# Performance work log

Hardware: AMD Instinct MI355X
Metric: run time of the kernel (lower is better)

## Reference

```python
import jax, jax.numpy as jnp
import numpy as np

N = 8192       # num nodes
F_IN = 256     # num_features
NHID = 128     # nhid
E = 524288     # num edges (avg degree 64)
K = 32         # num_edge_preseve


def setup_inputs() -> dict:
    key = jax.random.key(0)
    ks = jax.random.split(key, 5)
    x = jax.random.normal(ks[0], (N, F_IN), jnp.float32)
    edge_index = jax.random.randint(ks[1], (2, E), 0, N, jnp.int32)
    W1 = jax.random.normal(ks[2], (F_IN, NHID), jnp.float32) / np.sqrt(F_IN)
    b1 = jnp.zeros((NHID,), jnp.float32)
    We = jax.random.normal(ks[3], (2 * NHID, 1), jnp.float32) / np.sqrt(2 * NHID)
    be = jnp.zeros((1,), jnp.float32)
    return {"x": x, "edge_index": edge_index, "W1": W1, "b1": b1, "We": We, "be": be}


def _segment_sparsemax(z, seg, num_segments):
    """Sparsemax applied independently within each segment (row) of an edge list."""
    E_ = z.shape[0]
    # group edges by segment, descending score within segment
    order = jnp.lexsort((-z, seg))
    zs = z[order]
    ss = seg[order]
    counts = jnp.zeros((num_segments,), jnp.int32).at[seg].add(1)
    starts = jnp.cumsum(counts) - counts                 # first sorted index of each segment
    pos = jnp.arange(E_, dtype=jnp.int32) - starts[ss]   # 0-based rank within segment
    cs = jnp.cumsum(zs)
    prefix = cs - zs                                     # cumsum excluding self
    seg_cs = cs - prefix[starts][ss]                     # within-segment inclusive cumsum
    j1 = (pos + 1).astype(zs.dtype)
    cond = 1.0 + j1 * zs > seg_cs                        # sparsemax support condition
    kmax = jax.ops.segment_max(jnp.where(cond, pos + 1, 0), ss, num_segments=num_segments)
    kmax = jnp.maximum(kmax, 1)                          # nonempty segments always have k>=1
    idx = jnp.clip(starts + kmax - 1, 0, E_ - 1)
    seg_cs_at_k = cs[idx] - prefix[jnp.clip(starts, 0, E_ - 1)]
    tau = (seg_cs_at_k - 1.0) / kmax.astype(zs.dtype)
    out_sorted = jnp.maximum(zs - tau[ss], 0.0)
    return jnp.zeros_like(z).at[order].set(out_sorted)


def reference(x, edge_index, W1, b1, We, be):
    h = jax.nn.relu(x @ W1 + b1)                 # [N, NHID]
    row, col = edge_index[0], edge_index[1]
    # edge score: Linear on concat([h[row], h[col]]) == split matmul (avoids [E, 2*NHID] concat)
    e = h[row] @ We[:NHID, 0] + h[col] @ We[NHID:, 0] + be[0]   # [E]
    scores = _segment_sparsemax(e, row, N)       # row-segmented sparsemax
    adj = jnp.zeros((N, N), h.dtype).at[row, col].set(scores)
    topv = jax.lax.top_k(adj, K)[0]              # [N, K], sorted descending
    thresh = topv[:, -1:]                        # per-row k-th largest value
    new_adj = jnp.where(adj >= thresh, adj, jnp.zeros((), adj.dtype))
    # original returns dense_to_sparse(new_adj) (data-dependent shape);
    # we return the equivalent masked dense adjacency.
    return h, new_adj
```

## Files before the change

kernel.cpp:

```cpp
#include <hip/hip_runtime.h>

#define N_    8192
#define FIN_  256
#define NHID_ 128
#define E_    524288
#define KTOP  32
#define CAP   160
#define HASHSZ 512

typedef unsigned short ushort_t;

__global__ __launch_bounds__(256) void k_fused(const float* __restrict__ x,
                                               const int* __restrict__ ei,
                                               const float* __restrict__ W1,
                                               const float* __restrict__ b1,
                                               const float* __restrict__ We,
                                               float* __restrict__ h,
                                               float* __restrict__ a,
                                               float* __restrict__ b,
                                               int* __restrict__ cnt,
                                               ushort_t* __restrict__ ecol) {
    __shared__ float xs[16][FIN_];
    int t = threadIdx.x;
    int blk = blockIdx.x;

    {
        int4 r4 = ((const int4*)ei)[blk * 256 + t];
        int4 c4 = ((const int4*)(ei + E_))[blk * 256 + t];
        int p;
        p = atomicAdd(&cnt[r4.x], 1); if (p < CAP) ecol[r4.x * CAP + p] = (ushort_t)c4.x;
        p = atomicAdd(&cnt[r4.y], 1); if (p < CAP) ecol[r4.y * CAP + p] = (ushort_t)c4.y;
        p = atomicAdd(&cnt[r4.z], 1); if (p < CAP) ecol[r4.z * CAP + p] = (ushort_t)c4.z;
        p = atomicAdd(&cnt[r4.w], 1); if (p < CAP) ecol[r4.w * CAP + p] = (ushort_t)c4.w;
    }

    int row0 = blk * 16;
    const float4* xg = (const float4*)(x + (size_t)row0 * FIN_);
    float4* xs4 = (float4*)&xs[0][0];
#pragma unroll
    for (int i = 0; i < 4; ++i) xs4[t + 256 * i] = xg[t + 256 * i];
    __syncthreads();

    int rg = t >> 5;
    int jg = t & 31;
    int r0 = 2 * rg, r1 = 2 * rg + 1;
    const float* wp = W1 + jg * 4;
    float4 bb = *(const float4*)(b1 + jg * 4);
    float4 acc0 = bb, acc1 = bb;
    const float* xr0 = xs[r0];
    const float* xr1 = xs[r1];
#pragma unroll 8
    for (int k = 0; k < FIN_; ++k) {
        float4 w = *(const float4*)(wp + (size_t)k * NHID_);
        float x0 = xr0[k], x1 = xr1[k];
        acc0.x = fmaf(x0, w.x, acc0.x);
        acc0.y = fmaf(x0, w.y, acc0.y);
        acc0.z = fmaf(x0, w.z, acc0.z);
        acc0.w = fmaf(x0, w.w, acc0.w);
        acc1.x = fmaf(x1, w.x, acc1.x);
        acc1.y = fmaf(x1, w.y, acc1.y);
        acc1.z = fmaf(x1, w.z, acc1.z);
        acc1.w = fmaf(x1, w.w, acc1.w);
    }
    acc0.x = fmaxf(acc0.x, 0.f); acc0.y = fmaxf(acc0.y, 0.f);
    acc0.z = fmaxf(acc0.z, 0.f); acc0.w = fmaxf(acc0.w, 0.f);
    acc1.x = fmaxf(acc1.x, 0.f); acc1.y = fmaxf(acc1.y, 0.f);
    acc1.z = fmaxf(acc1.z, 0.f); acc1.w = fmaxf(acc1.w, 0.f);
    *(float4*)(h + (size_t)(row0 + r0) * NHID_ + jg * 4) = acc0;
    *(float4*)(h + (size_t)(row0 + r1) * NHID_ + jg * 4) = acc1;

    float4 we1 = *(const float4*)(We + jg * 4);
    float4 we2 = *(const float4*)(We + NHID_ + jg * 4);
    float p0 = acc0.x * we1.x + acc0.y * we1.y + acc0.z * we1.z + acc0.w * we1.w;
    float q0 = acc0.x * we2.x + acc0.y * we2.y + acc0.z * we2.z + acc0.w * we2.w;
    float p1 = acc1.x * we1.x + acc1.y * we1.y + acc1.z * we1.z + acc1.w * we1.w;
    float q1 = acc1.x * we2.x + acc1.y * we2.y + acc1.z * we2.z + acc1.w * we2.w;
#pragma unroll
    for (int o = 16; o > 0; o >>= 1) {
        p0 += __shfl_down(p0, o, 32);
        q0 += __shfl_down(q0, o, 32);
        p1 += __shfl_down(p1, o, 32);
        q1 += __shfl_down(q1, o, 32);
    }
    if (jg == 0) {
        a[row0 + r0] = p0; b[row0 + r0] = q0;
        a[row0 + r1] = p1; b[row0 + r1] = q1;
    }
}

__global__ __launch_bounds__(256) void k_rows(const int* __restrict__ cnt,
                                              const ushort_t* __restrict__ ecol,
                                              const float* __restrict__ a,
                                              const float* __restrict__ b,
                                              const float* __restrict__ be,
                                              float* __restrict__ adj) {
    __shared__ float zs[CAP];
    __shared__ int   cols[CAP];
    __shared__ float srt[CAP];
    __shared__ unsigned char dupf[CAP];
    __shared__ unsigned int bitmap[N_ / 32];
    __shared__ int   hcol[HASHSZ];
    __shared__ float hval[HASHSZ];
    __shared__ float s_tau, s_thresh;

    int r = blockIdx.x;
    int t = threadIdx.x;
    int m = cnt[r];
    if (m > CAP) m = CAP;

    bitmap[t] = 0u;
    hcol[t] = -1;
    hcol[t + 256] = -1;

    float ab = a[r] + be[0];
    for (int i = t; i < m; i += 256) {
        int c = (int)ecol[r * CAP + i];
        cols[i] = c;
        zs[i] = ab + b[c];
    }
    __syncthreads();

    if (m > 0) {
        for (int i = t; i < m; i += 256) {
            float zi = zs[i];
            int ci = cols[i];
            int rank = 0;
            for (int jj = 0; jj < m; ++jj) {
                float zj = zs[jj];
                rank += (zj > zi) || (zj == zi && jj < i);
            }
            bool dup = false;
            for (int jj = 0; jj < i; ++jj)
                if (cols[jj] == ci) { dup = true; break; }
            srt[rank] = zi;
            dupf[i] = dup ? 1 : 0;
        }
        __syncthreads();

        if (t == 0) {
            float c = 0.f;
            int kmax = 1;
            float csk = srt[0];
            for (int jj = 0; jj < m; ++jj) {
                c += srt[jj];
                if (1.0f + (float)(jj + 1) * srt[jj] > c) { kmax = jj + 1; csk = c; }
            }
            s_tau = (csk - 1.0f) / (float)kmax;
            s_thresh = 0.f;
        }
        __syncthreads();
        float tau = s_tau;

        for (int i = t; i < m; i += 256) {
            if (dupf[i]) continue;
            float zi = zs[i];
            int rank = 0;
            for (int jj = 0; jj < m; ++jj) {
                if (dupf[jj] || jj == i) continue;
                float zj = zs[jj];
                rank += (zj > zi) || (zj == zi && jj < i);
            }
            if (rank == KTOP - 1) {
                float s = zi - tau;
                s_thresh = s > 0.f ? s : 0.f;
            }
        }
        __syncthreads();
        float thresh = s_thresh;

        for (int i = t; i < m; i += 256) {
            if (dupf[i]) continue;
            float s = zs[i] - tau;
            if (s > 0.f && s >= thresh) {
                int c = cols[i];
                atomicOr(&bitmap[c >> 5], 1u << (c & 31));
                int slot = c & (HASHSZ - 1);
                while (atomicCAS(&hcol[slot], -1, c) != -1)
                    slot = (slot + 1) & (HASHSZ - 1);
                hval[slot] = s;
            }
        }
    }
    __syncthreads();

    float4* row4 = (float4*)(adj + (size_t)r * N_);
#pragma unroll
    for (int k2 = 0; k2 < 8; ++k2) {
        int idx = t + 256 * k2;
        unsigned int word = bitmap[idx >> 3];
        unsigned int nib = (word >> ((idx & 7) * 4)) & 0xFu;
        float4 v = make_float4(0.f, 0.f, 0.f, 0.f);
        if (nib) {
            int cbase = idx * 4;
#pragma unroll
            for (int bbit = 0; bbit < 4; ++bbit) {
                if (nib & (1u << bbit)) {
                    int c = cbase + bbit;
                    int slot = c & (HASHSZ - 1);
                    while (hcol[slot] != c) slot = (slot + 1) & (HASHSZ - 1);
                    float val = hval[slot];
                    if (bbit == 0) v.x = val;
                    else if (bbit == 1) v.y = val;
                    else if (bbit == 2) v.z = val;
                    else v.w = val;
                }
            }
        }
        row4[idx] = v;
    }
}

extern "C" void kernel_launch(void* const* d_in, const int* in_sizes, int n_in,
                              void* d_out, int out_size, void* d_ws, size_t ws_size,
                              hipStream_t stream) {
    const float* x  = (const float*)d_in[0];
    const int*   ei = (const int*)d_in[1];
    const float* W1 = (const float*)d_in[2];
    const float* b1 = (const float*)d_in[3];
    const float* We = (const float*)d_in[4];
    const float* be = (const float*)d_in[5];

    float* h_out   = (float*)d_out;
    float* adj_out = h_out + (size_t)N_ * NHID_;

    float*    a    = (float*)d_ws;
    float*    b    = a + N_;
    int*      cnt  = (int*)(b + N_);
    ushort_t* ecol = (ushort_t*)(cnt + N_);

    hipMemsetAsync(cnt, 0, N_ * sizeof(int), stream);
    k_fused<<<512, 256, 0, stream>>>(x, ei, W1, b1, We, h_out, a, b, cnt, ecol);
    k_rows <<<N_, 256, 0, stream>>>(cnt, ecol, a, b, be, adj_out);
}
```

Before: 371.1 us.

## Split row kernel into compact sparsemax compute and dense row write kernels

```diff
diff --git a/kernel.cpp b/kernel.cpp
--- a/kernel.cpp
+++ b/kernel.cpp
@@ -9,6 +9,7 @@
 #define HASHSZ 512
 
 typedef unsigned short ushort_t;
+typedef float v4f __attribute__((ext_vector_type(4)));
 
 __global__ __launch_bounds__(256) void k_fused(const float* __restrict__ x,
                                                const int* __restrict__ ei,
@@ -88,108 +89,130 @@
     }
 }
 
-__global__ __launch_bounds__(256) void k_rows(const int* __restrict__ cnt,
-                                              const ushort_t* __restrict__ ecol,
-                                              const float* __restrict__ a,
-                                              const float* __restrict__ b,
-                                              const float* __restrict__ be,
-                                              float* __restrict__ adj) {
+__global__ __launch_bounds__(64) void k_compute(const int* __restrict__ cnt,
+                                                const ushort_t* __restrict__ ecol,
+                                                const float* __restrict__ a,
+                                                const float* __restrict__ b,
+                                                const float* __restrict__ be,
+                                                int* __restrict__ kcnt,
+                                                ushort_t* __restrict__ kcol,
+                                                float* __restrict__ kval) {
     __shared__ float zs[CAP];
     __shared__ int   cols[CAP];
     __shared__ float srt[CAP];
     __shared__ unsigned char dupf[CAP];
-    __shared__ unsigned int bitmap[N_ / 32];
-    __shared__ int   hcol[HASHSZ];
-    __shared__ float hval[HASHSZ];
     __shared__ float s_tau, s_thresh;
+    __shared__ int   s_kc;
 
     int r = blockIdx.x;
     int t = threadIdx.x;
     int m = cnt[r];
     if (m > CAP) m = CAP;
+    if (m == 0) { if (t == 0) kcnt[r] = 0; return; }
+
+    if (t == 0) { s_kc = 0; s_thresh = 0.f; }
+    float ab = a[r] + be[0];
+    for (int i = t; i < m; i += 64) {
+        int c = (int)ecol[r * CAP + i];
+        cols[i] = c;
+        zs[i] = ab + b[c];
+    }
+    __syncthreads();
+
+    for (int i = t; i < m; i += 64) {
+        float zi = zs[i];
+        int ci = cols[i];
+        int rank = 0;
+        for (int jj = 0; jj < m; ++jj) {
+            float zj = zs[jj];
+            rank += (zj > zi) || (zj == zi && jj < i);
+        }
+        bool dup = false;
+        for (int jj = 0; jj < i; ++jj)
+            if (cols[jj] == ci) { dup = true; break; }
+        srt[rank] = zi;
+        dupf[i] = dup ? 1 : 0;
+    }
+    __syncthreads();
+
+    if (t == 0) {
+        float c = 0.f;
+        int kmax = 1;
+        float csk = srt[0];
+        for (int jj = 0; jj < m; ++jj) {
+            c += srt[jj];
+            if (1.0f + (float)(jj + 1) * srt[jj] > c) { kmax = jj + 1; csk = c; }
+        }
+        s_tau = (csk - 1.0f) / (float)kmax;
+    }
+    __syncthreads();
+    float tau = s_tau;
+
+    for (int i = t; i < m; i += 64) {
+        if (dupf[i]) continue;
+        float zi = zs[i];
+        int rank = 0;
+        for (int jj = 0; jj < m; ++jj) {
+            if (dupf[jj] || jj == i) continue;
+            float zj = zs[jj];
+            rank += (zj > zi) || (zj == zi && jj < i);
+        }
+        if (rank == KTOP - 1) {
+            float s = zi - tau;
+            s_thresh = s > 0.f ? s : 0.f;
+        }
+    }
+    __syncthreads();
+    float thresh = s_thresh;
+
+    for (int i = t; i < m; i += 64) {
+        if (dupf[i]) continue;
+        float s = zs[i] - tau;
+        if (s > 0.f && s >= thresh) {
+            int slot = atomicAdd(&s_kc, 1);
+            kcol[r * CAP + slot] = (ushort_t)cols[i];
+            kval[r * CAP + slot] = s;
+        }
+    }
+    __syncthreads();
+    if (t == 0) kcnt[r] = s_kc;
+}
+
+__global__ __launch_bounds__(256) void k_write(const int* __restrict__ kcnt,
+                                               const ushort_t* __restrict__ kcol,
+                                               const float* __restrict__ kval,
+                                               float* __restrict__ adj) {
+    __shared__ unsigned int bitmap[N_ / 32];
+    __shared__ int   hcol[HASHSZ];
+    __shared__ float hval[HASHSZ];
+
+    int r = blockIdx.x;
+    int t = threadIdx.x;
+    int kc = kcnt[r];
 
     bitmap[t] = 0u;
     hcol[t] = -1;
     hcol[t + 256] = -1;
-
-    float ab = a[r] + be[0];
-    for (int i = t; i < m; i += 256) {
-        int c = (int)ecol[r * CAP + i];
-        cols[i] = c;
-        zs[i] = ab + b[c];
-    }
-    __syncthreads();
-
-    if (m > 0) {
-        for (int i = t; i < m; i += 256) {
-            float zi = zs[i];
-            int ci = cols[i];
-            int rank = 0;
-            for (int jj = 0; jj < m; ++jj) {
-                float zj = zs[jj];
-                rank += (zj > zi) || (zj == zi && jj < i);
-            }
-            bool dup = false;
-            for (int jj = 0; jj < i; ++jj)
-                if (cols[jj] == ci) { dup = true; break; }
-            srt[rank] = zi;
-            dupf[i] = dup ? 1 : 0;
-        }
-        __syncthreads();
-
-        if (t == 0) {
-            float c = 0.f;
-            int kmax = 1;
-            float csk = srt[0];
-            for (int jj = 0; jj < m; ++jj) {
-                c += srt[jj];
-                if (1.0f + (float)(jj + 1) * srt[jj] > c) { kmax = jj + 1; csk = c; }
-            }
-            s_tau = (csk - 1.0f) / (float)kmax;
-            s_thresh = 0.f;
-        }
-        __syncthreads();
-        float tau = s_tau;
-
-        for (int i = t; i < m; i += 256) {
-            if (dupf[i]) continue;
-            float zi = zs[i];
-            int rank = 0;
-            for (int jj = 0; jj < m; ++jj) {
-                if (dupf[jj] || jj == i) continue;
-                float zj = zs[jj];
-                rank += (zj > zi) || (zj == zi && jj < i);
-            }
-            if (rank == KTOP - 1) {
-                float s = zi - tau;
-                s_thresh = s > 0.f ? s : 0.f;
-            }
-        }
-        __syncthreads();
-        float thresh = s_thresh;
-
-        for (int i = t; i < m; i += 256) {
-            if (dupf[i]) continue;
-            float s = zs[i] - tau;
-            if (s > 0.f && s >= thresh) {
-                int c = cols[i];
-                atomicOr(&bitmap[c >> 5], 1u << (c & 31));
-                int slot = c & (HASHSZ - 1);
-                while (atomicCAS(&hcol[slot], -1, c) != -1)
-                    slot = (slot + 1) & (HASHSZ - 1);
-                hval[slot] = s;
-            }
-        }
-    }
-    __syncthreads();
-
-    float4* row4 = (float4*)(adj + (size_t)r * N_);
+    __syncthreads();
+
+    for (int i = t; i < kc; i += 256) {
+        int c = (int)kcol[r * CAP + i];
+        float s = kval[r * CAP + i];
+        atomicOr(&bitmap[c >> 5], 1u << (c & 31));
+        int slot = c & (HASHSZ - 1);
+        while (atomicCAS(&hcol[slot], -1, c) != -1)
+            slot = (slot + 1) & (HASHSZ - 1);
+        hval[slot] = s;
+    }
+    __syncthreads();
+
+    v4f* row4 = (v4f*)(adj + (size_t)r * N_);
 #pragma unroll
     for (int k2 = 0; k2 < 8; ++k2) {
         int idx = t + 256 * k2;
         unsigned int word = bitmap[idx >> 3];
         unsigned int nib = (word >> ((idx & 7) * 4)) & 0xFu;
-        float4 v = make_float4(0.f, 0.f, 0.f, 0.f);
+        v4f v = (v4f)(0.f);
         if (nib) {
             int cbase = idx * 4;
 #pragma unroll
@@ -198,15 +221,11 @@
                     int c = cbase + bbit;
                     int slot = c & (HASHSZ - 1);
                     while (hcol[slot] != c) slot = (slot + 1) & (HASHSZ - 1);
-                    float val = hval[slot];
-                    if (bbit == 0) v.x = val;
-                    else if (bbit == 1) v.y = val;
-                    else if (bbit == 2) v.z = val;
-                    else v.w = val;
+                    v[bbit] = hval[slot];
                 }
             }
         }
-        row4[idx] = v;
+        __builtin_nontemporal_store(v, &row4[idx]);
     }
 }
 
@@ -226,9 +245,13 @@
     float*    a    = (float*)d_ws;
     float*    b    = a + N_;
     int*      cnt  = (int*)(b + N_);
-    ushort_t* ecol = (ushort_t*)(cnt + N_);
-
-    hipMemsetAsync(cnt, 0, N_ * sizeof(int), stream);
-    k_fused<<<512, 256, 0, stream>>>(x, ei, W1, b1, We, h_out, a, b, cnt, ecol);
-    k_rows <<<N_, 256, 0, stream>>>(cnt, ecol, a, b, be, adj_out);
-}
+    int*      kcnt = cnt + N_;
+    ushort_t* ecol = (ushort_t*)(kcnt + N_);
+    ushort_t* kcol = ecol + (size_t)N_ * CAP;
+    float*    kval = (float*)(kcol + (size_t)N_ * CAP);
+
+    (void)hipMemsetAsync(cnt, 0, N_ * sizeof(int), stream);
+    k_fused  <<<512, 256, 0, stream>>>(x, ei, W1, b1, We, h_out, a, b, cnt, ecol);
+    k_compute<<<N_, 64, 0, stream>>>(cnt, ecol, a, b, be, kcnt, kcol, kval);
+    k_write  <<<N_, 256, 0, stream>>>(kcnt, kcol, kval, adj_out);
+}
```

New measurement: 400.2 us. 1.08x slower.

## Compute per-row sparsemax and top-k threshold in one wavefront with shuffles

Applied to the files above, without the earlier changes.

```diff
diff --git a/kernel.cpp b/kernel.cpp
--- a/kernel.cpp
+++ b/kernel.cpp
@@ -97,11 +97,9 @@
     __shared__ float zs[CAP];
     __shared__ int   cols[CAP];
     __shared__ float srt[CAP];
-    __shared__ unsigned char dupf[CAP];
     __shared__ unsigned int bitmap[N_ / 32];
     __shared__ int   hcol[HASHSZ];
     __shared__ float hval[HASHSZ];
-    __shared__ float s_tau, s_thresh;
 
     int r = blockIdx.x;
     int t = threadIdx.x;
@@ -111,7 +109,6 @@
     bitmap[t] = 0u;
     hcol[t] = -1;
     hcol[t + 256] = -1;
-
     float ab = a[r] + be[0];
     for (int i = t; i < m; i += 256) {
         int c = (int)ecol[r * CAP + i];
@@ -120,63 +117,118 @@
     }
     __syncthreads();
 
-    if (m > 0) {
-        for (int i = t; i < m; i += 256) {
-            float zi = zs[i];
-            int ci = cols[i];
-            int rank = 0;
+    if (t < 64 && m > 0) {
+        int lane = t;
+        float z0 = (lane       < m) ? zs[lane]       : 0.f;
+        float z1 = (lane + 64  < m) ? zs[lane + 64]  : 0.f;
+        float z2 = (lane + 128 < m) ? zs[lane + 128] : 0.f;
+        int   c0 = (lane       < m) ? cols[lane]       : -1;
+        int   c1 = (lane + 64  < m) ? cols[lane + 64]  : -2;
+        int   c2 = (lane + 128 < m) ? cols[lane + 128] : -3;
+
+        int  r0 = 0, r1 = 0, r2 = 0;
+        bool d0 = false, d1 = false, d2 = false;
+        if (m <= 64) {
             for (int jj = 0; jj < m; ++jj) {
-                float zj = zs[jj];
-                rank += (zj > zi) || (zj == zi && jj < i);
-            }
-            bool dup = false;
-            for (int jj = 0; jj < i; ++jj)
-                if (cols[jj] == ci) { dup = true; break; }
-            srt[rank] = zi;
-            dupf[i] = dup ? 1 : 0;
-        }
-        __syncthreads();
-
-        if (t == 0) {
-            float c = 0.f;
-            int kmax = 1;
-            float csk = srt[0];
+                float zj = __shfl(z0, jj);
+                int   cj = __shfl(c0, jj);
+                r0 += (zj > z0) || (zj == z0 && jj < lane);
+                d0 = d0 || (cj == c0 && jj < lane);
+            }
+        } else {
             for (int jj = 0; jj < m; ++jj) {
-                c += srt[jj];
-                if (1.0f + (float)(jj + 1) * srt[jj] > c) { kmax = jj + 1; csk = c; }
-            }
-            s_tau = (csk - 1.0f) / (float)kmax;
-            s_thresh = 0.f;
-        }
-        __syncthreads();
-        float tau = s_tau;
-
-        for (int i = t; i < m; i += 256) {
-            if (dupf[i]) continue;
-            float zi = zs[i];
-            int rank = 0;
-            for (int jj = 0; jj < m; ++jj) {
-                if (dupf[jj] || jj == i) continue;
-                float zj = zs[jj];
-                rank += (zj > zi) || (zj == zi && jj < i);
-            }
-            if (rank == KTOP - 1) {
-                float s = zi - tau;
-                s_thresh = s > 0.f ? s : 0.f;
-            }
-        }
-        __syncthreads();
-        float thresh = s_thresh;
-
-        for (int i = t; i < m; i += 256) {
-            if (dupf[i]) continue;
-            float s = zs[i] - tau;
+                int slot = jj >> 6, lj = jj & 63;
+                float zj; int cj;
+                if (slot == 0)      { zj = __shfl(z0, lj); cj = __shfl(c0, lj); }
+                else if (slot == 1) { zj = __shfl(z1, lj); cj = __shfl(c1, lj); }
+                else                { zj = __shfl(z2, lj); cj = __shfl(c2, lj); }
+                int i1 = lane + 64, i2 = lane + 128;
+                r0 += (zj > z0) || (zj == z0 && jj < lane);
+                d0 = d0 || (cj == c0 && jj < lane);
+                r1 += (zj > z1) || (zj == z1 && jj < i1);
+                d1 = d1 || (cj == c1 && jj < i1);
+                r2 += (zj > z2) || (zj == z2 && jj < i2);
+                d2 = d2 || (cj == c2 && jj < i2);
+            }
+        }
+        if (lane       < m) srt[r0] = z0;
+        if (lane + 64  < m) srt[r1] = z1;
+        if (lane + 128 < m) srt[r2] = z2;
+
+        float v0 = (lane       < m) ? srt[lane]       : 0.f;
+        float v1 = (lane + 64  < m) ? srt[lane + 64]  : 0.f;
+        float v2 = (lane + 128 < m) ? srt[lane + 128] : 0.f;
+        float sc0 = v0, sc1 = v1, sc2 = v2;
+#pragma unroll
+        for (int o = 1; o < 64; o <<= 1) {
+            float u0 = __shfl_up(sc0, o);
+            float u1 = __shfl_up(sc1, o);
+            float u2 = __shfl_up(sc2, o);
+            if (lane >= o) { sc0 += u0; sc1 += u1; sc2 += u2; }
+        }
+        float tot0 = __shfl(sc0, 63);
+        sc1 += tot0;
+        float tot1 = __shfl(sc1, 63);
+        sc2 += tot1;
+        bool k0 = (lane       < m) && (1.f + (float)(lane + 1)   * v0 > sc0);
+        bool k1 = (lane + 64  < m) && (1.f + (float)(lane + 65)  * v1 > sc1);
+        bool k2 = (lane + 128 < m) && (1.f + (float)(lane + 129) * v2 > sc2);
+        unsigned long long b0 = __ballot(k0), b1 = __ballot(k1), b2 = __ballot(k2);
+        int kmax;
+        if (b2)      kmax = 128 + 63 - (int)__builtin_clzll(b2) + 1;
+        else if (b1) kmax = 64  + 63 - (int)__builtin_clzll(b1) + 1;
+        else         kmax =       63 - (int)__builtin_clzll(b0) + 1;
+        int ki = kmax - 1, ks = ki >> 6, kl = ki & 63;
+        float csk = (ks == 0) ? __shfl(sc0, kl) : (ks == 1) ? __shfl(sc1, kl) : __shfl(sc2, kl);
+        float tau = (csk - 1.f) / (float)kmax;
+
+        unsigned long long dm0 = __ballot(d0), dm1 = __ballot(d1), dm2 = __ballot(d2);
+        int u0 = 0, u1 = 0, u2 = 0;
+        for (int jj = 0; jj < m; ++jj) {
+            int slot = jj >> 6, lj = jj & 63;
+            unsigned long long dm = (slot == 0) ? dm0 : (slot == 1) ? dm1 : dm2;
+            if ((dm >> lj) & 1ull) continue;
+            float zj;
+            if (slot == 0)      zj = __shfl(z0, lj);
+            else if (slot == 1) zj = __shfl(z1, lj);
+            else                zj = __shfl(z2, lj);
+            u0 += (zj > z0) || (zj == z0 && jj < lane);
+            u1 += (zj > z1) || (zj == z1 && jj < lane + 64);
+            u2 += (zj > z2) || (zj == z2 && jj < lane + 128);
+        }
+        float cand = 0.f;
+        if (lane       < m && !d0 && u0 == KTOP - 1) cand = fmaxf(cand, fmaxf(z0 - tau, 0.f));
+        if (lane + 64  < m && !d1 && u1 == KTOP - 1) cand = fmaxf(cand, fmaxf(z1 - tau, 0.f));
+        if (lane + 128 < m && !d2 && u2 == KTOP - 1) cand = fmaxf(cand, fmaxf(z2 - tau, 0.f));
+#pragma unroll
+        for (int o = 32; o > 0; o >>= 1) cand = fmaxf(cand, __shfl_down(cand, o));
+        float thresh = __shfl(cand, 0);
+
+        float s;
+        if (lane < m && !d0) {
+            s = z0 - tau;
             if (s > 0.f && s >= thresh) {
-                int c = cols[i];
-                atomicOr(&bitmap[c >> 5], 1u << (c & 31));
-                int slot = c & (HASHSZ - 1);
-                while (atomicCAS(&hcol[slot], -1, c) != -1)
-                    slot = (slot + 1) & (HASHSZ - 1);
+                atomicOr(&bitmap[c0 >> 5], 1u << (c0 & 31));
+                int slot = c0 & (HASHSZ - 1);
+                while (atomicCAS(&hcol[slot], -1, c0) != -1) slot = (slot + 1) & (HASHSZ - 1);
+                hval[slot] = s;
+            }
+        }
+        if (lane + 64 < m && !d1) {
+            s = z1 - tau;
+            if (s > 0.f && s >= thresh) {
+                atomicOr(&bitmap[c1 >> 5], 1u << (c1 & 31));
+                int slot = c1 & (HASHSZ - 1);
+                while (atomicCAS(&hcol[slot], -1, c1) != -1) slot = (slot + 1) & (HASHSZ - 1);
+                hval[slot] = s;
+            }
+        }
+        if (lane + 128 < m && !d2) {
+            s = z2 - tau;
+            if (s > 0.f && s >= thresh) {
+                atomicOr(&bitmap[c2 >> 5], 1u << (c2 & 31));
+                int slot = c2 & (HASHSZ - 1);
+                while (atomicCAS(&hcol[slot], -1, c2) != -1) slot = (slot + 1) & (HASHSZ - 1);
                 hval[slot] = s;
             }
         }
@@ -228,7 +280,7 @@
     int*      cnt  = (int*)(b + N_);
     ushort_t* ecol = (ushort_t*)(cnt + N_);
 
-    hipMemsetAsync(cnt, 0, N_ * sizeof(int), stream);
+    (void)hipMemsetAsync(cnt, 0, N_ * sizeof(int), stream);
     k_fused<<<512, 256, 0, stream>>>(x, ei, W1, b1, We, h_out, a, b, cnt, ecol);
     k_rows <<<N_, 256, 0, stream>>>(cnt, ecol, a, b, be, adj_out);
 }
```

Result: slower. 395.9 us (+6.7%).

## Replace serial sparsemax scan and O(m^2) top-k rank pass with wavefront scan

Applied to the files above, without the earlier changes.

```diff
diff --git a/kernel.cpp b/kernel.cpp
--- a/kernel.cpp
+++ b/kernel.cpp
@@ -98,6 +98,7 @@
     __shared__ int   cols[CAP];
     __shared__ float srt[CAP];
     __shared__ unsigned char dupf[CAP];
+    __shared__ unsigned char dupsrt[CAP];
     __shared__ unsigned int bitmap[N_ / 32];
     __shared__ int   hcol[HASHSZ];
     __shared__ float hval[HASHSZ];
@@ -133,39 +134,61 @@
             for (int jj = 0; jj < i; ++jj)
                 if (cols[jj] == ci) { dup = true; break; }
             srt[rank] = zi;
+            dupsrt[rank] = dup ? 1 : 0;
             dupf[i] = dup ? 1 : 0;
         }
         __syncthreads();
 
-        if (t == 0) {
-            float c = 0.f;
-            int kmax = 1;
-            float csk = srt[0];
-            for (int jj = 0; jj < m; ++jj) {
-                c += srt[jj];
-                if (1.0f + (float)(jj + 1) * srt[jj] > c) { kmax = jj + 1; csk = c; }
-            }
-            s_tau = (csk - 1.0f) / (float)kmax;
-            s_thresh = 0.f;
+        if (t < 64) {
+            int lane = t;
+            float v0 = (lane       < m) ? srt[lane]       : 0.f;
+            float v1 = (lane + 64  < m) ? srt[lane + 64]  : 0.f;
+            float v2 = (lane + 128 < m) ? srt[lane + 128] : 0.f;
+            bool  d0 = (lane       < m) ? (dupsrt[lane]       != 0) : false;
+            bool  d1 = (lane + 64  < m) ? (dupsrt[lane + 64]  != 0) : false;
+            bool  d2 = (lane + 128 < m) ? (dupsrt[lane + 128] != 0) : false;
+
+            float sc0 = v0, sc1 = v1, sc2 = v2;
+#pragma unroll
+            for (int o = 1; o < 64; o <<= 1) {
+                float u0 = __shfl_up(sc0, o);
+                float u1 = __shfl_up(sc1, o);
+                float u2 = __shfl_up(sc2, o);
+                if (lane >= o) { sc0 += u0; sc1 += u1; sc2 += u2; }
+            }
+            float tot0 = __shfl(sc0, 63);
+            sc1 += tot0;
+            float tot1 = __shfl(sc1, 63);
+            sc2 += tot1;
+
+            bool k0 = (lane       < m) && (1.f + (float)(lane + 1)   * v0 > sc0);
+            bool k1 = (lane + 64  < m) && (1.f + (float)(lane + 65)  * v1 > sc1);
+            bool k2 = (lane + 128 < m) && (1.f + (float)(lane + 129) * v2 > sc2);
+            unsigned long long kb0 = __ballot(k0), kb1 = __ballot(k1), kb2 = __ballot(k2);
+            int kmax;
+            if (kb2)      kmax = 128 + 63 - (int)__builtin_clzll(kb2) + 1;
+            else if (kb1) kmax = 64  + 63 - (int)__builtin_clzll(kb1) + 1;
+            else          kmax =       63 - (int)__builtin_clzll(kb0) + 1;
+            int ki = kmax - 1, ks = ki >> 6, kl = ki & 63;
+            float csk = (ks == 0) ? __shfl(sc0, kl) : (ks == 1) ? __shfl(sc1, kl) : __shfl(sc2, kl);
+            float tau = (csk - 1.f) / (float)kmax;
+
+            unsigned long long dm0 = __ballot(d0), dm1 = __ballot(d1), dm2 = __ballot(d2);
+            unsigned long long below = (lane == 63) ? ~0ull >> 1 : ((1ull << lane) - 1ull);
+            below = (1ull << lane) - 1ull;
+            int pc0 = (int)__popcll(dm0 & below);
+            int pc1 = (int)__popcll(dm0) + (int)__popcll(dm1 & below);
+            int pc2 = (int)__popcll(dm0) + (int)__popcll(dm1) + (int)__popcll(dm2 & below);
+            float cand = 0.f;
+            if (lane       < m && !d0 && (lane       - pc0) == KTOP - 1) cand = fmaxf(cand, fmaxf(v0 - tau, 0.f));
+            if (lane + 64  < m && !d1 && (lane + 64  - pc1) == KTOP - 1) cand = fmaxf(cand, fmaxf(v1 - tau, 0.f));
+            if (lane + 128 < m && !d2 && (lane + 128 - pc2) == KTOP - 1) cand = fmaxf(cand, fmaxf(v2 - tau, 0.f));
+#pragma unroll
+            for (int o = 32; o > 0; o >>= 1) cand = fmaxf(cand, __shfl_down(cand, o));
+            if (lane == 0) { s_tau = tau; s_thresh = cand; }
         }
         __syncthreads();
         float tau = s_tau;
-
-        for (int i = t; i < m; i += 256) {
-            if (dupf[i]) continue;
-            float zi = zs[i];
-            int rank = 0;
-            for (int jj = 0; jj < m; ++jj) {
-                if (dupf[jj] || jj == i) continue;
-                float zj = zs[jj];
-                rank += (zj > zi) || (zj == zi && jj < i);
-            }
-            if (rank == KTOP - 1) {
-                float s = zi - tau;
-                s_thresh = s > 0.f ? s : 0.f;
-            }
-        }
-        __syncthreads();
         float thresh = s_thresh;
 
         for (int i = t; i < m; i += 256) {
@@ -228,7 +251,7 @@
     int*      cnt  = (int*)(b + N_);
     ushort_t* ecol = (ushort_t*)(cnt + N_);
 
-    hipMemsetAsync(cnt, 0, N_ * sizeof(int), stream);
+    (void)hipMemsetAsync(cnt, 0, N_ * sizeof(int), stream);
     k_fused<<<512, 256, 0, stream>>>(x, ei, W1, b1, We, h_out, a, b, cnt, ecol);
     k_rows <<<N_, 256, 0, stream>>>(cnt, ecol, a, b, be, adj_out);
 }
```

Measured after the change: 351.6 us. 1.06x faster.
